# Kernel optimization log

Hardware: AMD Instinct MI355X
Metric: run time of the kernel (lower is better)

The kernel has to match this reference:

```python
import jax, jax.numpy as jnp
import numpy as np

N, D, E, TOP_K = 4096, 1024, 8, 2
NEG_INF = -1e38


def setup_inputs() -> dict:
    key = jax.random.key(0)
    ks = jax.random.split(key, 6)
    s = 1.0 / np.sqrt(D)
    return {
        "x": jax.random.normal(ks[0], (N, D), jnp.float32),
        "noise": jax.random.normal(ks[1], (E,), jnp.float32),
        "Wg": jax.random.normal(ks[2], (D, E), jnp.float32) * s,
        "Wn": jax.random.normal(ks[3], (D, E), jnp.float32) * s,
        "We": jax.random.normal(ks[4], (E, D, D), jnp.float32) * s,
        "be": jax.random.normal(ks[5], (E, D), jnp.float32) * 0.01,
    }


def reference(x, noise, Wg, Wn, We, be):
    # Gating: H = Wg(x) + randn(E) * softplus(Wnoise(x))   (Eq. 4-5)
    g = x @ Wg                                      # [N, E]
    H = g + noise[None, :] * jax.nn.softplus(x @ Wn)  # [N, E]
    # Keep top_k entries of H, set the rest to -Inf (scatter of bottom E-k)
    vals, idx = jax.lax.top_k(H, TOP_K)             # [N, k]
    keep = jnp.full_like(H, NEG_INF)
    keep = keep.at[jnp.arange(H.shape[0])[:, None], idx].set(vals)
    G = jax.nn.softmax(keep, axis=1)                # [N, E]; masked entries -> 0
    # Expert outputs; masked experts have G==0 so dense weighted sum matches
    # the sparse per-example loop: out_n = sum_j G[n,j] * expert_j(x_n)
    Y = jnp.einsum('nd,edh->neh', x, We) + be[None, :, :]  # [N, E, D]
    out = jnp.einsum('ne,neh->nh', G, Y)            # [N, D]
    return out
```

## Files before the change

### kernel.cpp

```cpp
#include <hip/hip_runtime.h>
#include <hip/hip_bf16.h>
#include <stdint.h>

#define NR   4096
#define DIM  1024
#define NE   8
#define BM   128
#define BN   128
#define BK2  32

typedef __attribute__((ext_vector_type(8))) short  bf16x8;
typedef __attribute__((ext_vector_type(8))) ushort u16x8;
typedef __attribute__((ext_vector_type(4))) float  f32x4;

__device__ __forceinline__ ushort f2bf(float f) {
    union { __hip_bfloat16 h; ushort u; } cv;
    cv.h = __float2bfloat16(f);
    return cv.u;
}

__device__ __forceinline__ void gload16(const void* g, void* l) {
    __builtin_amdgcn_global_load_lds(
        (const __attribute__((address_space(1))) unsigned int*)g,
        (__attribute__((address_space(3))) unsigned int*)l, 16, 0, 0);
}

__global__ __launch_bounds__(256)
void k1_prep(const float* __restrict__ Wg, const float* __restrict__ Wn,
             float* __restrict__ WT, float* __restrict__ out) {
    const int tid = threadIdx.x;
    if (blockIdx.x < 8) {
        const int k    = blockIdx.x * 128 + (tid >> 1);
        const int half = tid & 1;
        const float* src = half ? Wn : Wg;
        const float4* s4 = (const float4*)(src + (size_t)k * NE);
        float4 a = s4[0], b = s4[1];
        float* d = WT + (size_t)half * 8 * DIM;
        d[(size_t)0 * DIM + k] = a.x; d[(size_t)1 * DIM + k] = a.y;
        d[(size_t)2 * DIM + k] = a.z; d[(size_t)3 * DIM + k] = a.w;
        d[(size_t)4 * DIM + k] = b.x; d[(size_t)5 * DIM + k] = b.y;
        d[(size_t)6 * DIM + k] = b.z; d[(size_t)7 * DIM + k] = b.w;
    } else {
        const int vb = blockIdx.x - 8;
        float4 z = {0.f, 0.f, 0.f, 0.f};
        for (int i = vb * 256 + tid; i < NR * DIM / 4; i += 512 * 256)
            ((float4*)out)[i] = z;
    }
}

__global__ __launch_bounds__(256)
void k2_main(const float* __restrict__ We, ushort* __restrict__ WeT,
             const float* __restrict__ x, const float* __restrict__ noise,
             const float* __restrict__ WT, ushort* __restrict__ xbf,
             uint32_t* __restrict__ eid, float2* __restrict__ wpair) {
    __shared__ float smem[64 * 68];
    const int tid = threadIdx.x;
    if (blockIdx.x < 2048) {
        const int b  = blockIdx.x;
        const int e  = b >> 8, kt = (b >> 4) & 15, ct = b & 15;
        const float* src = We + ((size_t)e * DIM + (size_t)kt * 64) * DIM + ct * 64;
#pragma unroll
        for (int j = 0; j < 4; ++j) {
            int idx = tid + j * 256;
            int r = idx >> 4, c4 = idx & 15;
            *(float4*)&smem[r * 68 + c4 * 4] = *(const float4*)(src + (size_t)r * DIM + c4 * 4);
        }
        __syncthreads();
        ushort* dst = WeT + ((size_t)e * DIM + (size_t)ct * 64) * DIM + kt * 64;
#pragma unroll
        for (int j = 0; j < 2; ++j) {
            int u = tid + j * 256;
            int c = u >> 3, ch = u & 7;
            ushort tmp[8];
#pragma unroll
            for (int q = 0; q < 8; ++q) tmp[q] = f2bf(smem[(ch * 8 + q) * 68 + c]);
            *(u16x8*)(dst + (size_t)c * DIM + ch * 8) = *(u16x8*)tmp;
        }
    } else {
        const int w = tid >> 6, l = tid & 63;
        const int row = (blockIdx.x - 2048) * 4 + w;
        const float* xr = x + (size_t)row * DIM;

        float4 xv[4];
#pragma unroll
        for (int q = 0; q < 4; ++q) xv[q] = *(const float4*)(xr + q * 256 + l * 4);
#pragma unroll
        for (int q = 0; q < 4; ++q) {
            ushort4 xb;
            xb.x = f2bf(xv[q].x); xb.y = f2bf(xv[q].y);
            xb.z = f2bf(xv[q].z); xb.w = f2bf(xv[q].w);
            *(ushort4*)(xbf + (size_t)row * DIM + q * 256 + l * 4) = xb;
        }

        float acc[16];
#pragma unroll
        for (int u = 0; u < 16; ++u) {
            const float* wr_ = WT + (size_t)u * DIM + l * 4;
            float s = 0.f;
#pragma unroll
            for (int q = 0; q < 4; ++q) {
                float4 wv = *(const float4*)(wr_ + q * 256);
                s += xv[q].x * wv.x + xv[q].y * wv.y + xv[q].z * wv.z + xv[q].w * wv.w;
            }
            acc[u] = s;
        }
#pragma unroll
        for (int u = 0; u < 16; ++u) smem[(w * 64 + l) * 17 + u] = acc[u];
        asm volatile("s_waitcnt lgkmcnt(0)" ::: "memory");
        const int c = l >> 4, u = l & 15;
        float v = 0.f;
#pragma unroll
        for (int i = 0; i < 16; ++i) v += smem[(w * 64 + c * 16 + i) * 17 + u];
        v += __shfl_xor(v, 16, 64);
        v += __shfl_xor(v, 32, 64);

        const int e = l & 7;
        float ag = __shfl(v, e, 64);
        float an = __shfl(v, e + 8, 64);
        float sp = (an > 0.f) ? (an + log1pf(expf(-an))) : log1pf(expf(an));
        float H  = ag + noise[e] * sp;

        float Hh[8];
#pragma unroll
        for (int k = 0; k < 8; ++k) Hh[k] = __shfl(H, k, 64);
        if (l == 0) {
            int e0 = 0; float v0 = Hh[0];
#pragma unroll
            for (int k = 1; k < 8; ++k) if (Hh[k] > v0) { v0 = Hh[k]; e0 = k; }
            int e1 = -1; float v1 = 0.f;
#pragma unroll
            for (int k = 0; k < 8; ++k)
                if (k != e0 && (e1 < 0 || Hh[k] > v1)) { v1 = Hh[k]; e1 = k; }
            float rr = expf(v1 - v0);
            float w0 = 1.f / (1.f + rr), w1 = 1.f - w0;
            eid[row] = (uint32_t)e0 | ((uint32_t)e1 << 8);
            float2 wp; wp.x = w0; wp.y = w1;
            wpair[row] = wp;
        }
    }
}

__global__ __launch_bounds__(1024)
void bucket_build(const uint32_t* __restrict__ eid, const float2* __restrict__ wpair,
                  int* __restrict__ cnt, int* __restrict__ idxl, float* __restrict__ wl) {
    const int bucket = blockIdx.x;
    const int slot = bucket >> 3, ex = bucket & 7;
    __shared__ int base;
    __shared__ int wsum[16];
    if (threadIdx.x == 0) base = 0;
    const int wid = threadIdx.x >> 6, lane = threadIdx.x & 63;
    int* bidx = idxl + (size_t)bucket * NR;
    float* bwl = wl + (size_t)bucket * NR;

    for (int c0 = 0; c0 < NR; c0 += 1024) {
        const int row = c0 + threadIdx.x;
        const uint32_t em = eid[row];
        const int e = slot ? (int)((em >> 8) & 255u) : (int)(em & 255u);
        const bool m = (e == ex);
        const unsigned long long bal = __ballot(m);
        if (lane == 0) wsum[wid] = __popcll(bal);
        __syncthreads();
        int wbase = base;
        for (int i = 0; i < wid; ++i) wbase += wsum[i];
        const int pos = wbase + __popcll(bal & ((1ull << lane) - 1ull));
        if (m) {
            bidx[pos] = row;
            float2 wp = wpair[row];
            bwl[pos]  = slot ? wp.y : wp.x;
        }
        __syncthreads();
        if (threadIdx.x == 0) {
            int s = 0;
#pragma unroll
            for (int i = 0; i < 16; ++i) s += wsum[i];
            base += s;
        }
        __syncthreads();
    }
    if (threadIdx.x == 0) cnt[bucket] = base;
}

__global__ __launch_bounds__(256, 4)
void moe_gemm(const ushort* __restrict__ xbf, const ushort* __restrict__ WeT,
              const float* __restrict__ be, const int* __restrict__ cnt,
              const int* __restrict__ idxl, const float* __restrict__ wl,
              float* __restrict__ out) {
    __shared__ ushort Al[2][BM][BK2];
    __shared__ ushort Bl[2][BM][BK2];

    const int q8 = gridDim.x >> 3;
    const int W  = (blockIdx.x & 7) * q8 + (blockIdx.x >> 3);
    const int bucket = W >> 8;
    const int t  = (W >> 3) & 31;
    const int cT = W & 7;
    const int count = cnt[bucket];
    if (t * BM >= count) return;
    const int nrowsv = min(BM, count - t * BM);
    const int e  = bucket & 7;
    const int c0 = cT * BN;
    const int*   rows = idxl + (size_t)bucket * NR + t * BM;
    const float* wrow = wl   + (size_t)bucket * NR + t * BM;

    const int tid = threadIdx.x, wid = tid >> 6, lane = tid & 63;
    const int wr = (wid >> 1) * 64, wc = (wid & 1) * 64;
    const int l16 = lane & 15, lhi = lane >> 4;

    const int srow = lane >> 2;
    const int sch  = ((lane & 3) ^ ((lane >> 3) & 3)) * 8;
    const ushort* aptr[2];
    const ushort* bptr[2];
#pragma unroll
    for (int q = 0; q < 2; ++q) {
        int r = wid * 32 + q * 16 + srow;
        aptr[q] = xbf + (size_t)rows[min(r, nrowsv - 1)] * DIM + sch;
        int c = c0 + wid * 32 + q * 16 + srow;
        bptr[q] = WeT + ((size_t)(e * DIM + c)) * DIM + sch;
    }

    f32x4 acc[4][4];
#pragma unroll
    for (int m = 0; m < 4; ++m)
#pragma unroll
        for (int n = 0; n < 4; ++n) { f32x4 z = {0.f, 0.f, 0.f, 0.f}; acc[m][n] = z; }

#pragma unroll
    for (int q = 0; q < 2; ++q) {
        gload16(aptr[q], &Al[0][wid * 32 + q * 16][0]);
        gload16(bptr[q], &Bl[0][wid * 32 + q * 16][0]);
    }

    const int chb = (lhi ^ ((l16 >> 1) & 3)) * 8;
    const int NSTEP = DIM / BK2;
    for (int s = 0; s < NSTEP; ++s) {
        const int buf = s & 1;
        if (s + 1 < NSTEP) {
            const int nb = buf ^ 1, k0 = (s + 1) * BK2;
#pragma unroll
            for (int q = 0; q < 2; ++q) {
                gload16(aptr[q] + k0, &Al[nb][wid * 32 + q * 16][0]);
                gload16(bptr[q] + k0, &Bl[nb][wid * 32 + q * 16][0]);
            }
            asm volatile("s_waitcnt vmcnt(4)" ::: "memory");
        } else {
            asm volatile("s_waitcnt vmcnt(0)" ::: "memory");
        }
        __builtin_amdgcn_s_barrier();

        const ushort* Ab = &Al[buf][0][0];
        const ushort* Bb = &Bl[buf][0][0];
        bf16x8 af[4], bfr[4];
#pragma unroll
        for (int m = 0; m < 4; ++m)
            af[m] = *(const bf16x8*)(Ab + (wr + m * 16 + l16) * BK2 + chb);
#pragma unroll
        for (int n = 0; n < 4; ++n)
            bfr[n] = *(const bf16x8*)(Bb + (wc + n * 16 + l16) * BK2 + chb);
#pragma unroll
        for (int m = 0; m < 4; ++m)
#pragma unroll
            for (int n = 0; n < 4; ++n)
                acc[m][n] = __builtin_amdgcn_mfma_f32_16x16x32_bf16(af[m], bfr[n], acc[m][n], 0, 0, 0);

        asm volatile("s_waitcnt lgkmcnt(0)" ::: "memory");
        __builtin_amdgcn_s_barrier();
    }

    float bev[4];
#pragma unroll
    for (int n = 0; n < 4; ++n) bev[n] = be[(size_t)e * DIM + c0 + wc + n * 16 + l16];
#pragma unroll
    for (int m = 0; m < 4; ++m) {
#pragma unroll
        for (int r = 0; r < 4; ++r) {
            int rl = wr + m * 16 + lhi * 4 + r;
            if (rl < nrowsv) {
                int   gr = rows[rl];
                float w  = wrow[rl];
                float* op = out + (size_t)gr * DIM + c0 + wc;
#pragma unroll
                for (int n = 0; n < 4; ++n)
                    atomicAdd(&op[n * 16 + l16], w * (acc[m][n][r] + bev[n]));
            }
        }
    }
}

extern "C" void kernel_launch(void* const* d_in, const int* in_sizes, int n_in,
                              void* d_out, int out_size, void* d_ws, size_t ws_size,
                              hipStream_t stream) {
    const float* x     = (const float*)d_in[0];
    const float* noise = (const float*)d_in[1];
    const float* Wg    = (const float*)d_in[2];
    const float* Wn    = (const float*)d_in[3];
    const float* We    = (const float*)d_in[4];
    const float* be    = (const float*)d_in[5];
    float* out = (float*)d_out;

    char* w = (char*)d_ws;
    size_t off = 256;
    int*      cnt   = (int*)w;
    int*      idxl  = (int*)(w + off);      off += (size_t)2 * NE * NR * 4;
    float*    wl    = (float*)(w + off);    off += (size_t)2 * NE * NR * 4;
    uint32_t* eid   = (uint32_t*)(w + off); off += (size_t)NR * 4;
    float2*   wpair = (float2*)(w + off);   off += (size_t)NR * 8;
    off = (off + 255) & ~(size_t)255;
    float*  WT  = (float*)(w + off);  off += (size_t)16 * DIM * 4;
    ushort* xbf = (ushort*)(w + off); off += (size_t)NR * DIM * 2;
    ushort* WeT = (ushort*)(w + off); off += (size_t)NE * DIM * DIM * 2;

    k1_prep<<<520, 256, 0, stream>>>(Wg, Wn, WT, out);
    k2_main<<<3072, 256, 0, stream>>>(We, WeT, x, noise, WT, xbf, eid, wpair);
    bucket_build<<<16, 1024, 0, stream>>>(eid, wpair, cnt, idxl, wl);
    moe_gemm<<<16 * 32 * 8, 256, 0, stream>>>(xbf, WeT, be, cnt, idxl, wl, out);
}
```

Before: 89.87 us.

## Shrink MoE GEMM row tile, deepen K step, and compact the tile grid

```diff
diff --git a/kernel.cpp b/kernel.cpp
--- a/kernel.cpp
+++ b/kernel.cpp
@@ -5,9 +5,9 @@
 #define NR   4096
 #define DIM  1024
 #define NE   8
-#define BM   128
+#define BM   64
 #define BN   128
-#define BK2  32
+#define BK   64
 
 typedef __attribute__((ext_vector_type(8))) short  bf16x8;
 typedef __attribute__((ext_vector_type(8))) ushort u16x8;
@@ -180,87 +180,93 @@
     if (threadIdx.x == 0) cnt[bucket] = base;
 }
 
-__global__ __launch_bounds__(256, 4)
+__global__ __launch_bounds__(256, 3)
 void moe_gemm(const ushort* __restrict__ xbf, const ushort* __restrict__ WeT,
               const float* __restrict__ be, const int* __restrict__ cnt,
               const int* __restrict__ idxl, const float* __restrict__ wl,
               float* __restrict__ out) {
-    __shared__ ushort Al[2][BM][BK2];
-    __shared__ ushort Bl[2][BM][BK2];
+    __shared__ ushort Al[2][BM][BK];
+    __shared__ ushort Bl[2][BN][BK];
 
     const int q8 = gridDim.x >> 3;
     const int W  = (blockIdx.x & 7) * q8 + (blockIdx.x >> 3);
-    const int bucket = W >> 8;
-    const int t  = (W >> 3) & 31;
-    const int cT = W & 7;
-    const int count = cnt[bucket];
-    if (t * BM >= count) return;
-    const int nrowsv = min(BM, count - t * BM);
+    const int item = W >> 3, cT = W & 7;
+
+    int bucket = -1, tile = 0, accp = 0;
+#pragma unroll
+    for (int b = 0; b < 16; ++b) {
+        int t = (cnt[b] + BM - 1) >> 6;
+        if (bucket < 0 && item < accp + t) { bucket = b; tile = item - accp; }
+        accp += t;
+    }
+    if (bucket < 0) return;
+    const int count  = cnt[bucket];
+    const int nrowsv = min(BM, count - tile * BM);
     const int e  = bucket & 7;
     const int c0 = cT * BN;
-    const int*   rows = idxl + (size_t)bucket * NR + t * BM;
-    const float* wrow = wl   + (size_t)bucket * NR + t * BM;
+    const int*   rows = idxl + (size_t)bucket * NR + tile * BM;
+    const float* wrow = wl   + (size_t)bucket * NR + tile * BM;
 
     const int tid = threadIdx.x, wid = tid >> 6, lane = tid & 63;
-    const int wr = (wid >> 1) * 64, wc = (wid & 1) * 64;
+    const int wr = (wid >> 1) * 32, wc = (wid & 1) * 64;
     const int l16 = lane & 15, lhi = lane >> 4;
 
-    const int srow = lane >> 2;
-    const int sch  = ((lane & 3) ^ ((lane >> 3) & 3)) * 8;
+    const int schunk = ((lane & 7) ^ ((lane >> 3) & 7)) * 8;
     const ushort* aptr[2];
-    const ushort* bptr[2];
+    const ushort* bptr[4];
 #pragma unroll
     for (int q = 0; q < 2; ++q) {
-        int r = wid * 32 + q * 16 + srow;
-        aptr[q] = xbf + (size_t)rows[min(r, nrowsv - 1)] * DIM + sch;
-        int c = c0 + wid * 32 + q * 16 + srow;
-        bptr[q] = WeT + ((size_t)(e * DIM + c)) * DIM + sch;
-    }
-
-    f32x4 acc[4][4];
-#pragma unroll
-    for (int m = 0; m < 4; ++m)
+        int r = q * 32 + wid * 8 + (lane >> 3);
+        aptr[q] = xbf + (size_t)rows[min(r, nrowsv - 1)] * DIM + schunk;
+    }
+#pragma unroll
+    for (int q = 0; q < 4; ++q) {
+        int c = c0 + q * 32 + wid * 8 + (lane >> 3);
+        bptr[q] = WeT + ((size_t)(e * DIM + c)) * DIM + schunk;
+    }
+
+    f32x4 acc[2][4];
+#pragma unroll
+    for (int m = 0; m < 2; ++m)
 #pragma unroll
         for (int n = 0; n < 4; ++n) { f32x4 z = {0.f, 0.f, 0.f, 0.f}; acc[m][n] = z; }
 
 #pragma unroll
-    for (int q = 0; q < 2; ++q) {
-        gload16(aptr[q], &Al[0][wid * 32 + q * 16][0]);
-        gload16(bptr[q], &Bl[0][wid * 32 + q * 16][0]);
-    }
-
-    const int chb = (lhi ^ ((l16 >> 1) & 3)) * 8;
-    const int NSTEP = DIM / BK2;
+    for (int q = 0; q < 2; ++q) gload16(aptr[q], &Al[0][q * 32 + wid * 8][0]);
+#pragma unroll
+    for (int q = 0; q < 4; ++q) gload16(bptr[q], &Bl[0][q * 32 + wid * 8][0]);
+
+    const int NSTEP = DIM / BK;
     for (int s = 0; s < NSTEP; ++s) {
         const int buf = s & 1;
         if (s + 1 < NSTEP) {
-            const int nb = buf ^ 1, k0 = (s + 1) * BK2;
-#pragma unroll
-            for (int q = 0; q < 2; ++q) {
-                gload16(aptr[q] + k0, &Al[nb][wid * 32 + q * 16][0]);
-                gload16(bptr[q] + k0, &Bl[nb][wid * 32 + q * 16][0]);
-            }
-            asm volatile("s_waitcnt vmcnt(4)" ::: "memory");
+            const int nb = buf ^ 1, k0 = (s + 1) * BK;
+#pragma unroll
+            for (int q = 0; q < 2; ++q) gload16(aptr[q] + k0, &Al[nb][q * 32 + wid * 8][0]);
+#pragma unroll
+            for (int q = 0; q < 4; ++q) gload16(bptr[q] + k0, &Bl[nb][q * 32 + wid * 8][0]);
+            asm volatile("s_waitcnt vmcnt(6)" ::: "memory");
         } else {
             asm volatile("s_waitcnt vmcnt(0)" ::: "memory");
         }
         __builtin_amdgcn_s_barrier();
 
-        const ushort* Ab = &Al[buf][0][0];
-        const ushort* Bb = &Bl[buf][0][0];
-        bf16x8 af[4], bfr[4];
-#pragma unroll
-        for (int m = 0; m < 4; ++m)
-            af[m] = *(const bf16x8*)(Ab + (wr + m * 16 + l16) * BK2 + chb);
-#pragma unroll
-        for (int n = 0; n < 4; ++n)
-            bfr[n] = *(const bf16x8*)(Bb + (wc + n * 16 + l16) * BK2 + chb);
-#pragma unroll
-        for (int m = 0; m < 4; ++m)
+#pragma unroll
+        for (int h = 0; h < 2; ++h) {
+            const int slot = ((h * 4 + lhi) ^ (l16 & 7)) * 8;
+            bf16x8 af[2], bfr[4];
+#pragma unroll
+            for (int m = 0; m < 2; ++m)
+                af[m] = *(const bf16x8*)(&Al[buf][wr + m * 16 + l16][0] + slot);
 #pragma unroll
             for (int n = 0; n < 4; ++n)
-                acc[m][n] = __builtin_amdgcn_mfma_f32_16x16x32_bf16(af[m], bfr[n], acc[m][n], 0, 0, 0);
-
+                bfr[n] = *(const bf16x8*)(&Bl[buf][wc + n * 16 + l16][0] + slot);
+#pragma unroll
+            for (int m = 0; m < 2; ++m)
+#pragma unroll
+                for (int n = 0; n < 4; ++n)
+                    acc[m][n] = __builtin_amdgcn_mfma_f32_16x16x32_bf16(af[m], bfr[n], acc[m][n], 0, 0, 0);
+        }
         asm volatile("s_waitcnt lgkmcnt(0)" ::: "memory");
         __builtin_amdgcn_s_barrier();
     }
@@ -269,7 +275,7 @@
 #pragma unroll
     for (int n = 0; n < 4; ++n) bev[n] = be[(size_t)e * DIM + c0 + wc + n * 16 + l16];
 #pragma unroll
-    for (int m = 0; m < 4; ++m) {
+    for (int m = 0; m < 2; ++m) {
 #pragma unroll
         for (int r = 0; r < 4; ++r) {
             int rl = wr + m * 16 + lhi * 4 + r;
@@ -311,5 +317,5 @@
     k1_prep<<<520, 256, 0, stream>>>(Wg, Wn, WT, out);
     k2_main<<<3072, 256, 0, stream>>>(We, WeT, x, noise, WT, xbf, eid, wpair);
     bucket_build<<<16, 1024, 0, stream>>>(eid, wpair, cnt, idxl, wl);
-    moe_gemm<<<16 * 32 * 8, 256, 0, stream>>>(xbf, WeT, be, cnt, idxl, wl, out);
-}
+    moe_gemm<<<144 * 8, 256, 0, stream>>>(xbf, WeT, be, cnt, idxl, wl, out);
+}
```

Result: faster. 87.05 us (-3.1%).

## Triple-buffer MoE GEMM LDS pipeline and compact tile grid over active buckets

Applied to the files above, without the earlier changes.

```diff
diff --git a/kernel.cpp b/kernel.cpp
--- a/kernel.cpp
+++ b/kernel.cpp
@@ -7,7 +7,7 @@
 #define NE   8
 #define BM   128
 #define BN   128
-#define BK2  32
+#define BK   32
 
 typedef __attribute__((ext_vector_type(8))) short  bf16x8;
 typedef __attribute__((ext_vector_type(8))) ushort u16x8;
@@ -180,41 +180,48 @@
     if (threadIdx.x == 0) cnt[bucket] = base;
 }
 
-__global__ __launch_bounds__(256, 4)
+__global__ __launch_bounds__(256, 3)
 void moe_gemm(const ushort* __restrict__ xbf, const ushort* __restrict__ WeT,
               const float* __restrict__ be, const int* __restrict__ cnt,
               const int* __restrict__ idxl, const float* __restrict__ wl,
               float* __restrict__ out) {
-    __shared__ ushort Al[2][BM][BK2];
-    __shared__ ushort Bl[2][BM][BK2];
+    __shared__ ushort lds[3][256][BK];
 
     const int q8 = gridDim.x >> 3;
     const int W  = (blockIdx.x & 7) * q8 + (blockIdx.x >> 3);
-    const int bucket = W >> 8;
-    const int t  = (W >> 3) & 31;
-    const int cT = W & 7;
-    const int count = cnt[bucket];
-    if (t * BM >= count) return;
-    const int nrowsv = min(BM, count - t * BM);
+    const int item = W >> 3, cT = W & 7;
+
+    int bucket = -1, tile = 0, accp = 0;
+#pragma unroll
+    for (int b = 0; b < 16; ++b) {
+        int t = (cnt[b] + BM - 1) >> 7;
+        if (bucket < 0 && item < accp + t) { bucket = b; tile = item - accp; }
+        accp += t;
+    }
+    if (bucket < 0) return;
+    const int count  = cnt[bucket];
+    const int nrowsv = min(BM, count - tile * BM);
     const int e  = bucket & 7;
     const int c0 = cT * BN;
-    const int*   rows = idxl + (size_t)bucket * NR + t * BM;
-    const float* wrow = wl   + (size_t)bucket * NR + t * BM;
+    const int*   rows = idxl + (size_t)bucket * NR + tile * BM;
+    const float* wrow = wl   + (size_t)bucket * NR + tile * BM;
 
     const int tid = threadIdx.x, wid = tid >> 6, lane = tid & 63;
+    const int l16 = lane & 15, lhi = lane >> 4;
     const int wr = (wid >> 1) * 64, wc = (wid & 1) * 64;
-    const int l16 = lane & 15, lhi = lane >> 4;
-
-    const int srow = lane >> 2;
-    const int sch  = ((lane & 3) ^ ((lane >> 3) & 3)) * 8;
+
+    const int lr   = lane >> 2;
+    const int fs   = ((lane >> 2) ^ (lane >> 4)) & 3;
+    const int csrc = ((lane & 3) ^ fs) * 8;
     const ushort* aptr[2];
     const ushort* bptr[2];
 #pragma unroll
-    for (int q = 0; q < 2; ++q) {
-        int r = wid * 32 + q * 16 + srow;
-        aptr[q] = xbf + (size_t)rows[min(r, nrowsv - 1)] * DIM + sch;
-        int c = c0 + wid * 32 + q * 16 + srow;
-        bptr[q] = WeT + ((size_t)(e * DIM + c)) * DIM + sch;
+    for (int p = 0; p < 2; ++p) {
+        int ridx = p * 64 + wid * 16 + lr;
+        int gr   = rows[min(ridx, nrowsv - 1)];
+        aptr[p]  = xbf + (size_t)gr * DIM + csrc;
+        int col  = c0 + p * 64 + wid * 16 + lr;
+        bptr[p]  = WeT + ((size_t)(e * DIM + col)) * DIM + csrc;
     }
 
     f32x4 acc[4][4];
@@ -223,47 +230,55 @@
 #pragma unroll
         for (int n = 0; n < 4; ++n) { f32x4 z = {0.f, 0.f, 0.f, 0.f}; acc[m][n] = z; }
 
-#pragma unroll
-    for (int q = 0; q < 2; ++q) {
-        gload16(aptr[q], &Al[0][wid * 32 + q * 16][0]);
-        gload16(bptr[q], &Bl[0][wid * 32 + q * 16][0]);
-    }
-
-    const int chb = (lhi ^ ((l16 >> 1) & 3)) * 8;
-    const int NSTEP = DIM / BK2;
-    for (int s = 0; s < NSTEP; ++s) {
-        const int buf = s & 1;
-        if (s + 1 < NSTEP) {
-            const int nb = buf ^ 1, k0 = (s + 1) * BK2;
-#pragma unroll
-            for (int q = 0; q < 2; ++q) {
-                gload16(aptr[q] + k0, &Al[nb][wid * 32 + q * 16][0]);
-                gload16(bptr[q] + k0, &Bl[nb][wid * 32 + q * 16][0]);
-            }
+#define STAGE(T, BUF) do {                                                   \
+    const int _k0 = (T) * BK;                                                \
+    ushort* _b = &lds[(BUF)][0][0];                                          \
+    _Pragma("unroll")                                                        \
+    for (int p = 0; p < 2; ++p) {                                            \
+        gload16(aptr[p] + _k0, _b + (p * 64 + wid * 16) * BK);               \
+        gload16(bptr[p] + _k0, _b + (128 + p * 64 + wid * 16) * BK);         \
+    }                                                                        \
+} while (0)
+
+    const int fr    = (l16 ^ (l16 >> 2)) & 3;
+    const int rslot = (lhi ^ fr) * 8;
+
+    const int NS = DIM / BK;
+    STAGE(0, 0);
+    STAGE(1, 1);
+    int c = 0, s = 2;
+    for (int t = 0; t < NS; ++t) {
+        if (t + 2 < NS) {
+            STAGE(t + 2, s);
+            asm volatile("s_waitcnt vmcnt(8)" ::: "memory");
+        } else if (t + 1 < NS) {
             asm volatile("s_waitcnt vmcnt(4)" ::: "memory");
         } else {
             asm volatile("s_waitcnt vmcnt(0)" ::: "memory");
         }
         __builtin_amdgcn_s_barrier();
 
-        const ushort* Ab = &Al[buf][0][0];
-        const ushort* Bb = &Bl[buf][0][0];
+        const ushort* base = &lds[c][0][0];
         bf16x8 af[4], bfr[4];
 #pragma unroll
         for (int m = 0; m < 4; ++m)
-            af[m] = *(const bf16x8*)(Ab + (wr + m * 16 + l16) * BK2 + chb);
+            af[m] = *(const bf16x8*)(base + (wr + m * 16 + l16) * BK + rslot);
 #pragma unroll
         for (int n = 0; n < 4; ++n)
-            bfr[n] = *(const bf16x8*)(Bb + (wc + n * 16 + l16) * BK2 + chb);
+            bfr[n] = *(const bf16x8*)(base + (128 + wc + n * 16 + l16) * BK + rslot);
+        __builtin_amdgcn_s_setprio(1);
 #pragma unroll
         for (int m = 0; m < 4; ++m)
 #pragma unroll
             for (int n = 0; n < 4; ++n)
                 acc[m][n] = __builtin_amdgcn_mfma_f32_16x16x32_bf16(af[m], bfr[n], acc[m][n], 0, 0, 0);
+        __builtin_amdgcn_s_setprio(0);
 
         asm volatile("s_waitcnt lgkmcnt(0)" ::: "memory");
         __builtin_amdgcn_s_barrier();
-    }
+        s = c; c = (c == 2) ? 0 : c + 1;
+    }
+#undef STAGE
 
     float bev[4];
 #pragma unroll
@@ -311,5 +326,5 @@
     k1_prep<<<520, 256, 0, stream>>>(Wg, Wn, WT, out);
     k2_main<<<3072, 256, 0, stream>>>(We, WeT, x, noise, WT, xbf, eid, wpair);
     bucket_build<<<16, 1024, 0, stream>>>(eid, wpair, cnt, idxl, wl);
-    moe_gemm<<<16 * 32 * 8, 256, 0, stream>>>(xbf, WeT, be, cnt, idxl, wl, out);
-}
+    moe_gemm<<<80 * 8, 256, 0, stream>>>(xbf, WeT, be, cnt, idxl, wl, out);
+}
```

Result: faster. 85.38 us (-5.0%).
